# Kernel tuning notes

Measured on AMD Instinct MI355X. Metric: run time of the kernel, lower is better.

Reference implementation:

```python
import jax, jax.numpy as jnp
import numpy as np

EPS = 1e-5


def _instance_norm(a):
    # InstanceNorm2d(affine=False): normalize each [*, ch] plane over last two dims
    mu = jnp.mean(a, axis=(-2, -1), keepdims=True)
    var = jnp.var(a, axis=(-2, -1), keepdims=True)  # biased, matches torch
    return (a - mu) * jax.lax.rsqrt(var + EPS)


def setup_inputs() -> dict:
    key = jax.random.key(0)
    ks = jax.random.split(key, 10)
    B, N, C, H = 8, 4096, 128, 8
    HC = C * H
    s = 0.02
    return {
        "emb": jax.random.normal(ks[0], (B, N, C), jnp.float32),
        "wq_uu": jax.random.normal(ks[1], (HC, C), jnp.float32) * s,
        "wk_uu": jax.random.normal(ks[2], (HC, C), jnp.float32) * s,
        "wv_uu": jax.random.normal(ks[3], (HC, C), jnp.float32) * s,
        "wq_lu": jax.random.normal(ks[4], (HC, C), jnp.float32) * s,
        "wk_lu": jax.random.normal(ks[5], (HC, C), jnp.float32) * s,
        "wv_lu": jax.random.normal(ks[6], (HC, C), jnp.float32) * s,
        "wo_u": jax.random.normal(ks[7], (C, HC), jnp.float32) * s,
        "wo_l": jax.random.normal(ks[8], (C, HC), jnp.float32) * s,
    }


def reference(emb, wq_uu, wk_uu, wv_uu, wq_lu, wk_lu, wv_lu, wo_u, wo_l):
    B, N, C = emb.shape
    HC = wq_uu.shape[0]
    H = HC // C
    b = B // 2
    emb_l, emb_u = emb[:b], emb[b:]

    def heads(x, w):  # [b,N,C] @ [HC,C]^T -> [b,H,N,C]
        return (x @ w.T).reshape(b, N, H, C).transpose(0, 2, 1, 3)

    # ---- branch u_u: channel attention within unlabeled half ----
    Q = heads(emb_u, wq_uu)  # [b,H,N,C]
    K = heads(emb_u, wk_uu)  # [b,H,N,C]
    V = heads(emb_u, wv_uu)  # [b,H,N,C]
    attn = jnp.einsum('bhnc,bhnd->bhcd', Q, K)          # Q^T K : [b,H,C,C]
    sim = jax.nn.softmax(_instance_norm(attn), axis=3)
    ctx = jnp.einsum('bhcd,bhnd->bhcn', sim, V)         # [b,H,C,N]
    # permute(0,3,2,1) then flatten (C,H) -> c-major, h-minor
    ctx = ctx.transpose(0, 3, 2, 1).reshape(b, N, HC)
    O_u = ctx @ wo_u.T                                   # [b,N,C]

    # ---- branch l_u: labeled queries attend over concat-of-batch unlabeled K/V ----
    Q2 = emb_l @ wq_lu.T                                 # [b,N,HC]
    K2 = (emb_u @ wk_lu.T).transpose(1, 0, 2).reshape(N, b * HC)  # 'b n c -> n (b c)'
    V2 = (emb_u @ wv_lu.T).transpose(1, 0, 2).reshape(N, b * HC)
    attn2 = jnp.einsum('bnc,nd->bcd', Q2, K2)            # [b,HC,b*HC] (single head)
    sim2 = jax.nn.softmax(_instance_norm(attn2), axis=2)
    ctx2 = jnp.einsum('bcd,nd->bnc', sim2, V2)           # [b,N,HC]
    O_l = ctx2 @ wo_l.T                                  # [b,N,C]

    return jnp.concatenate([O_l, O_u], axis=0)
```

## Files before the change

kernel.cpp:

```cpp
#include <hip/hip_runtime.h>
#include <hip/hip_bf16.h>

using bf16 = __hip_bfloat16;
typedef __attribute__((ext_vector_type(8))) short bf16x8;
typedef __attribute__((ext_vector_type(4))) float f32x4;

static __device__ __forceinline__ void storeC(float* p, float v) { *p = v; }
static __device__ __forceinline__ void storeC(bf16* p, float v) { *p = __float2bfloat16(v); }

static __device__ __forceinline__ void gl2lds16(const bf16* g, bf16* l)
{
    __builtin_amdgcn_global_load_lds(
        (const __attribute__((address_space(1))) unsigned int*)g,
        (__attribute__((address_space(3))) unsigned int*)l, 16, 0, 0);
}

static __device__ __forceinline__ void stage_tile(const bf16* gtile, int ld, bf16* ltile, int w, int lane)
{
    const bf16* g0 = gtile + (long)(w * 32 + (lane >> 2)) * ld + ((lane & 3) << 3);
    gl2lds16(g0, ltile + (w * 32) * 32);
    gl2lds16(g0 + (long)16 * ld, ltile + (w * 32 + 16) * 32);
}

template <typename TC, bool ATOMIC>
__global__ __launch_bounds__(256) void gemm_mfma_nt(
    const bf16* __restrict__ A0, const bf16* __restrict__ B0, TC* __restrict__ C0,
    int K, int lda, int ldb, int ldc, int zdiv,
    long sAhi, long sAlo, long sBhi, long sBlo, long sChi, long sClo)
{
    __shared__ bf16 As[2][4096];
    __shared__ bf16 Bs[2][4096];
    const int z = blockIdx.z;
    const bf16* A = A0 + (long)(z / zdiv) * sAhi + (long)(z % zdiv) * sAlo + (long)blockIdx.y * 128 * lda;
    const bf16* B = B0 + (long)(z / zdiv) * sBhi + (long)(z % zdiv) * sBlo + (long)blockIdx.x * 128 * ldb;
    TC*       C = C0 + (long)(z / zdiv) * sChi + (long)(z % zdiv) * sClo;

    const int t = threadIdx.x, lane = t & 63, w = t >> 6;
    const int wm = w >> 1, wn = w & 1;

    f32x4 acc[4][4] = {};

    stage_tile(A, lda, &As[0][0], w, lane);
    stage_tile(B, ldb, &Bs[0][0], w, lane);

    const int KT = K >> 5;
    for (int kt = 0; kt < KT; ++kt) {
        __syncthreads();
        const int cur = kt & 1;
        if (kt + 1 < KT) {
            stage_tile(A + (kt + 1) * 32, lda, &As[cur ^ 1][0], w, lane);
            stage_tile(B + (kt + 1) * 32, ldb, &Bs[cur ^ 1][0], w, lane);
        }
        const int kofs = (lane >> 4) << 3;
        bf16x8 av[4], bv[4];
#pragma unroll
        for (int i = 0; i < 4; ++i)
            av[i] = *(const bf16x8*)&As[cur][(wm * 64 + i * 16 + (lane & 15)) * 32 + kofs];
#pragma unroll
        for (int j = 0; j < 4; ++j)
            bv[j] = *(const bf16x8*)&Bs[cur][(wn * 64 + j * 16 + (lane & 15)) * 32 + kofs];
#pragma unroll
        for (int i = 0; i < 4; ++i)
#pragma unroll
            for (int j = 0; j < 4; ++j)
                acc[i][j] = __builtin_amdgcn_mfma_f32_16x16x32_bf16(av[i], bv[j], acc[i][j], 0, 0, 0);
    }

    const int r0 = blockIdx.y * 128 + wm * 64;
    const int c0 = blockIdx.x * 128 + wn * 64;
    const int lcol = lane & 15, lrow = (lane >> 4) << 2;
#pragma unroll
    for (int i = 0; i < 4; ++i)
#pragma unroll
        for (int j = 0; j < 4; ++j) {
            const int row = r0 + i * 16 + lrow;
            const int col = c0 + j * 16 + lcol;
#pragma unroll
            for (int r = 0; r < 4; ++r) {
                if constexpr (ATOMIC)
                    atomicAdd(&C[(long)(row + r) * ldc + col], acc[i][j][r]);
                else
                    storeC(&C[(long)(row + r) * ldc + col], acc[i][j][r]);
            }
        }
}

template <typename TC, bool STATS>
__global__ __launch_bounds__(512, 2) void gemm_mfma_nt256(
    const bf16* __restrict__ A0, const bf16* __restrict__ B0, TC* __restrict__ C0,
    int K, int lda, int ldb, int ldc, long sA, long sB, long sC, float* __restrict__ red)
{
    extern __shared__ bf16 lds[];
    const int z = blockIdx.z;
    const bf16* A = A0 + (long)z * sA + (long)blockIdx.y * 256 * lda;
    const bf16* B = B0 + (long)z * sB + (long)blockIdx.x * 256 * ldb;
    TC*       C = C0 + (long)z * sC;

    const int t = threadIdx.x, lane = t & 63, w = t >> 6;
    const int wm = w >> 2, wn = w & 3;
    const int lr = lane & 15, lg = lane >> 4;

    f32x4 acc[8][4] = {};
    const int KT = K >> 5;

    const int srow = t >> 2, spc = t & 3;
    auto STAGE_A = [&](int c) {
        bf16* base = lds + (c & 3) * 16384;
        const bf16* Ag = A + c * 32;
        const int r0 = srow, r1 = srow + 128;
        gl2lds16(Ag + (long)r0 * lda + ((spc ^ ((r0 >> 1) & 3)) << 3), base + w * 512);
        gl2lds16(Ag + (long)r1 * lda + ((spc ^ ((r1 >> 1) & 3)) << 3), base + 4096 + w * 512);
    };
    auto STAGE_B = [&](int c) {
        bf16* base = lds + (c & 3) * 16384 + 8192;
        const bf16* Bg = B + c * 32;
        const int r0 = srow, r1 = srow + 128;
        gl2lds16(Bg + (long)r0 * ldb + ((spc ^ ((r0 >> 1) & 3)) << 3), base + w * 512);
        gl2lds16(Bg + (long)r1 * ldb + ((spc ^ ((r1 >> 1) & 3)) << 3), base + 4096 + w * 512);
    };

    if (KT > 0) { STAGE_A(0); STAGE_B(0); }
    if (KT > 1) { STAGE_A(1); STAGE_B(1); }
    if (KT > 2) { STAGE_A(2); STAGE_B(2); }

    for (int c = 0; c < KT; ++c) {
        const int rem = KT - 1 - c;
        if (rem >= 2)      asm volatile("s_waitcnt vmcnt(8)" ::: "memory");
        else if (rem == 1) asm volatile("s_waitcnt vmcnt(4)" ::: "memory");
        else               asm volatile("s_waitcnt vmcnt(0)" ::: "memory");
        __builtin_amdgcn_s_barrier();
        asm volatile("" ::: "memory");

        const bf16* Ab = lds + (c & 3) * 16384;
        const bf16* Bb = Ab + 8192;
        const bool pf = (c + 3 < KT);

        bf16x8 bfrag[4], afragA[4];
#pragma unroll
        for (int j = 0; j < 4; ++j) {
            const int r = wn * 64 + j * 16 + lr;
            bfrag[j] = *(const bf16x8*)&Bb[r * 32 + ((lg ^ ((r >> 1) & 3)) << 3)];
        }
#pragma unroll
        for (int i = 0; i < 4; ++i) {
            const int r = wm * 128 + i * 16 + lr;
            afragA[i] = *(const bf16x8*)&Ab[r * 32 + ((lg ^ ((r >> 1) & 3)) << 3)];
        }
        if (pf) STAGE_A(c + 3);
        __builtin_amdgcn_s_barrier();
        __builtin_amdgcn_s_setprio(1);
#pragma unroll
        for (int i = 0; i < 4; ++i)
#pragma unroll
            for (int j = 0; j < 4; ++j)
                acc[i][j] = __builtin_amdgcn_mfma_f32_16x16x32_bf16(afragA[i], bfrag[j], acc[i][j], 0, 0, 0);
        __builtin_amdgcn_s_setprio(0);
        __builtin_amdgcn_s_barrier();

        bf16x8 afragB[4];
#pragma unroll
        for (int i = 0; i < 4; ++i) {
            const int r = wm * 128 + (4 + i) * 16 + lr;
            afragB[i] = *(const bf16x8*)&Ab[r * 32 + ((lg ^ ((r >> 1) & 3)) << 3)];
        }
        if (pf) STAGE_B(c + 3);
        __builtin_amdgcn_s_barrier();
        __builtin_amdgcn_s_setprio(1);
#pragma unroll
        for (int i = 0; i < 4; ++i)
#pragma unroll
            for (int j = 0; j < 4; ++j)
                acc[4 + i][j] = __builtin_amdgcn_mfma_f32_16x16x32_bf16(afragB[i], bfrag[j], acc[4 + i][j], 0, 0, 0);
        __builtin_amdgcn_s_setprio(0);
        __builtin_amdgcn_s_barrier();
    }

    const int r0 = blockIdx.y * 256 + wm * 128 + (lg << 2);
    const int c0 = blockIdx.x * 256 + wn * 64 + lr;
#pragma unroll
    for (int i = 0; i < 8; ++i)
#pragma unroll
        for (int j = 0; j < 4; ++j) {
#pragma unroll
            for (int rr = 0; rr < 4; ++rr)
                storeC(&C[(long)(r0 + i * 16 + rr) * ldc + (c0 + j * 16)], acc[i][j][rr]);
        }

    if constexpr (STATS) {
        float s1 = 0.f, s2 = 0.f;
#pragma unroll
        for (int i = 0; i < 8; ++i)
#pragma unroll
            for (int j = 0; j < 4; ++j)
#pragma unroll
                for (int rr = 0; rr < 4; ++rr) {
                    float v = acc[i][j][rr];
                    s1 += v; s2 += v * v;
                }
#pragma unroll
        for (int o = 32; o > 0; o >>= 1) { s1 += __shfl_xor(s1, o); s2 += __shfl_xor(s2, o); }
        __syncthreads();
        float* rb = (float*)lds;
        if (lane == 0) { rb[w] = s1; rb[8 + w] = s2; }
        __syncthreads();
        if (t == 0) {
            float a = 0.f, b = 0.f;
#pragma unroll
            for (int i = 0; i < 8; ++i) { a += rb[i]; b += rb[8 + i]; }
            atomicAdd(&red[z * 2], a);
            atomicAdd(&red[z * 2 + 1], b);
        }
    }
}

__global__ __launch_bounds__(256) void prep(
    const float* __restrict__ emb,
    const float* w0, const float* w1, const float* w2, const float* w3,
    const float* w4, const float* w5, const float* w6,
    const float* __restrict__ wo_u,
    bf16* __restrict__ embB, bf16* __restrict__ wB, bf16* __restrict__ woUrB,
    float* __restrict__ attnU, float* __restrict__ red2)
{
    const int b = blockIdx.x;
    if (b < 2048 || (b >= 2048 && b < 2496)) {
        const float* in;
        bf16* out;
        int i;
        if (b < 2048) {
            in = emb; out = embB;
            i = (b * 256 + threadIdx.x) * 8;
        } else {
            const int sub = b - 2048;
            const float* srcs[7] = {w0, w1, w2, w3, w4, w5, w6};
            in = srcs[sub >> 6];
            out = wB + (long)(sub >> 6) * 131072;
            i = ((sub & 63) * 256 + threadIdx.x) * 8;
        }
        float4 a = *(const float4*)(in + i);
        float4 c = *(const float4*)(in + i + 4);
        union { bf16 h[8]; uint4 u; } pk;
        pk.h[0] = __float2bfloat16(a.x); pk.h[1] = __float2bfloat16(a.y);
        pk.h[2] = __float2bfloat16(a.z); pk.h[3] = __float2bfloat16(a.w);
        pk.h[4] = __float2bfloat16(c.x); pk.h[5] = __float2bfloat16(c.y);
        pk.h[6] = __float2bfloat16(c.z); pk.h[7] = __float2bfloat16(c.w);
        *(uint4*)(out + i) = pk.u;
    } else if (b < 3008) {
        int i = (b - 2496) * 256 + threadIdx.x;
        int j = i >> 10, col = i & 1023;
        int h = col >> 7, cc = col & 127;
        woUrB[i] = __float2bfloat16(wo_u[j * 1024 + cc * 8 + h]);
    } else if (b < 3520) {
        int i = ((b - 3008) * 256 + threadIdx.x) * 4;
        *(float4*)(attnU + i) = float4{0.f, 0.f, 0.f, 0.f};
    } else {
        if (threadIdx.x < 8) red2[threadIdx.x] = 0.f;
    }
}

__global__ __launch_bounds__(256) void stats_bh(const float* __restrict__ x, float* __restrict__ stats)
{
    const float* p = x + (long)blockIdx.x * 16384;
    float s1 = 0.f, s2 = 0.f;
    for (int i = threadIdx.x; i < 16384; i += 256) { float v = p[i]; s1 += v; s2 += v * v; }
    __shared__ float r1[256], r2[256];
    int t = threadIdx.x;
    r1[t] = s1; r2[t] = s2; __syncthreads();
    for (int o = 128; o > 0; o >>= 1) {
        if (t < o) { r1[t] += r1[t + o]; r2[t] += r2[t + o]; }
        __syncthreads();
    }
    if (t == 0) {
        float mu = r1[0] * (1.f / 16384.f);
        float var = r2[0] * (1.f / 16384.f) - mu * mu;
        stats[blockIdx.x * 2] = mu;
        stats[blockIdx.x * 2 + 1] = rsqrtf(var + 1e-5f);
    }
}

__global__ __launch_bounds__(128) void softmax_row128(const float* __restrict__ attn,
                                                      const float* __restrict__ stats,
                                                      bf16* __restrict__ out)
{
    const int row = blockIdx.x;
    const int bh = row >> 7;
    const float mu = stats[bh * 2], rs = stats[bh * 2 + 1];
    const float* p = attn + (long)row * 128;
    const int t = threadIdx.x;
    float x = (p[t] - mu) * rs;
    float m = x;
#pragma unroll
    for (int o = 32; o > 0; o >>= 1) m = fmaxf(m, __shfl_xor(m, o));
    __shared__ float sm[2], ss[2];
    if ((t & 63) == 0) sm[t >> 6] = m;
    __syncthreads();
    m = fmaxf(sm[0], sm[1]);
    float e = expf(x - m);
    float s = e;
#pragma unroll
    for (int o = 32; o > 0; o >>= 1) s += __shfl_xor(s, o);
    if ((t & 63) == 0) ss[t >> 6] = s;
    __syncthreads();
    s = ss[0] + ss[1];
    out[(long)row * 128 + t] = __float2bfloat16(e / s);
}

__global__ __launch_bounds__(256) void softmax_row4096(const float* __restrict__ attn2,
                                                       const float* __restrict__ red,
                                                       bf16* __restrict__ out)
{
    const int row = blockIdx.x;
    const int b = row >> 10;
    const float inv = 1.f / 4194304.f;
    float mu = red[b * 2] * inv;
    float var = red[b * 2 + 1] * inv - mu * mu;
    float rs = rsqrtf(var + 1e-5f);
    const float* p = attn2 + (long)row * 4096;
    bf16* q = out + (long)row * 4096;
    const int t = threadIdx.x;
    float v[16];
    float mx = -3.0e38f;
#pragma unroll
    for (int i = 0; i < 16; ++i) { float u = (p[i * 256 + t] - mu) * rs; v[i] = u; mx = fmaxf(mx, u); }
#pragma unroll
    for (int o = 32; o > 0; o >>= 1) mx = fmaxf(mx, __shfl_xor(mx, o));
    __shared__ float sm[4], ss[4];
    if ((t & 63) == 0) sm[t >> 6] = mx;
    __syncthreads();
    mx = fmaxf(fmaxf(sm[0], sm[1]), fmaxf(sm[2], sm[3]));
    float s = 0.f;
#pragma unroll
    for (int i = 0; i < 16; ++i) { v[i] = expf(v[i] - mx); s += v[i]; }
#pragma unroll
    for (int o = 32; o > 0; o >>= 1) s += __shfl_xor(s, o);
    if ((t & 63) == 0) ss[t >> 6] = s;
    __syncthreads();
    s = ss[0] + ss[1] + ss[2] + ss[3];
    float r = 1.f / s;
#pragma unroll
    for (int i = 0; i < 16; ++i) q[i * 256 + t] = __float2bfloat16(v[i] * r);
}

extern "C" void kernel_launch(void* const* d_in, const int* in_sizes, int n_in,
                              void* d_out, int out_size, void* d_ws, size_t ws_size,
                              hipStream_t stream)
{
    const float* emb   = (const float*)d_in[0];
    const float* wq_uu = (const float*)d_in[1];
    const float* wk_uu = (const float*)d_in[2];
    const float* wv_uu = (const float*)d_in[3];
    const float* wq_lu = (const float*)d_in[4];
    const float* wk_lu = (const float*)d_in[5];
    const float* wv_lu = (const float*)d_in[6];
    const float* wo_u  = (const float*)d_in[7];
    const float* wo_l  = (const float*)d_in[8];
    float* out = (float*)d_out;

    hipFuncSetAttribute(reinterpret_cast<const void*>(&gemm_mfma_nt256<float, true>),
                        hipFuncAttributeMaxDynamicSharedMemorySize, 131072);
    hipFuncSetAttribute(reinterpret_cast<const void*>(&gemm_mfma_nt256<bf16, false>),
                        hipFuncAttributeMaxDynamicSharedMemorySize, 131072);

    const long U = 16777216;
    bf16*  ws     = (bf16*)d_ws;
    bf16*  slot0  = ws;
    bf16*  slot1  = ws + U;
    float* attn2F = (float*)(ws + 2 * U);
    float* attnU  = attn2F;
    bf16*  VuB    = (bf16*)attn2F;
    bf16*  ctx2B  = (bf16*)attn2F;
    bf16*  embB   = ws + 4 * U;
    bf16*  wB     = embB + 4194304;
    bf16*  wqUU  = wB;
    bf16*  wqLU  = wB + 262144;
    bf16*  wvUU  = wB + 524288;
    bf16*  wvLU  = wB + 655360;
    bf16*  woLB  = wB + 786432;
    bf16*  woUrB = wB + 917504;
    bf16*  simU   = wB + 1048576;
    float* statsF = (float*)(simU + 524288);
    float* statsU = statsF;
    float* red2   = statsF + 64;
    bf16*  ctxUB  = (bf16*)(statsF + 128);

    bf16* embB_l = embB;
    bf16* embB_u = embB + 2097152;

    dim3 blk(256);

    prep<<<dim3(3521), blk, 0, stream>>>(
        emb, wq_uu, wk_uu, wq_lu, wk_lu, wv_uu, wv_lu, wo_l, wo_u,
        embB, wB, woUrB, attnU, red2);

    gemm_mfma_nt<bf16, false><<<dim3(32, 8, 8), blk, 0, stream>>>(
        wqUU, embB_u, slot0, 128, 128, 128, 4096,
        4, 131072, 0, 0, 524288, 16777216, 4194304);

    gemm_mfma_nt<float, true><<<dim3(1, 1, 256), blk, 0, stream>>>(
        slot0, slot1, attnU, 512, 4096, 4096, 128,
        8, 524288, 512, 524288, 512, 16384, 0);

    stats_bh<<<dim3(32), blk, 0, stream>>>(attnU, statsU);
    softmax_row128<<<dim3(4096), dim3(128), 0, stream>>>(attnU, statsU, simU);

    gemm_mfma_nt<bf16, false><<<dim3(8, 32, 4), blk, 0, stream>>>(
        embB_u, wvUU, VuB, 128, 128, 128, 1024, 1, 524288, 0, 0, 0, 4194304, 0);

    gemm_mfma_nt<bf16, false><<<dim3(1, 32, 32), blk, 0, stream>>>(
        VuB, simU, ctxUB, 128, 1024, 128, 1024,
        8, 4194304, 128, 131072, 16384, 4194304, 128);

    gemm_mfma_nt<bf16, false><<<dim3(32, 8, 8), blk, 0, stream>>>(
        wqLU, embB_l, slot0, 128, 128, 128, 4096,
        4, 131072, 0, 2097152, 524288, 16777216, 4194304);

    gemm_mfma_nt256<float, true><<<dim3(16, 4, 4), dim3(512), 131072, stream>>>(
        slot0, slot1, attn2F, 4096, 4096, 4096, 4096,
        4194304, 0, 4194304, red2);

    softmax_row4096<<<dim3(4096), blk, 0, stream>>>(attn2F, red2, slot0);

    gemm_mfma_nt<bf16, false><<<dim3(8, 32, 4), blk, 0, stream>>>(
        embB_u, wvLU, slot1, 128, 128, 128, 4096, 1, 524288, 0, 0, 0, 1024, 0);

    gemm_mfma_nt256<bf16, false><<<dim3(4, 16, 4), dim3(512), 131072, stream>>>(
        slot1, slot0, ctx2B, 4096, 4096, 4096, 1024,
        0, 4194304, 4194304, nullptr);

    gemm_mfma_nt<float, false><<<dim3(1, 128, 2), blk, 0, stream>>>(
        ctx2B, woLB, out, 1024, 1024, 1024, 128,
        1, (long)(ctxUB - ctx2B), 0, 131072, 0, 2097152, 0);
}
```

Baseline: 500.5 us.

## Reassociate output projection through softmax matrices and fuse softmax stages

The output projections are reassociated: Wo·sim is computed first as small weight-sized products (W2u, W2l), so the large ctx2 GEMM over N×HC is replaced by a V·W2 product with split-K partials summed in a reduce kernel. The u-branch stats and softmax are merged into one kernel that also writes a transposed sim. The l-branch softmax is split into row-stats and transposed-write kernels. The 256 GEMM pipeline is simplified to one combined A/B stage per iteration with fewer barriers. The aim is to cut the FLOPs and memory traffic of the ctx2 path, at the cost of extra kernels and an added partial-sum reduction.

```diff
diff --git a/kernel.cpp b/kernel.cpp
--- a/kernel.cpp
+++ b/kernel.cpp
@@ -104,24 +104,22 @@
     const int KT = K >> 5;
 
     const int srow = t >> 2, spc = t & 3;
-    auto STAGE_A = [&](int c) {
+    auto STAGE = [&](int c) {
         bf16* base = lds + (c & 3) * 16384;
         const bf16* Ag = A + c * 32;
-        const int r0 = srow, r1 = srow + 128;
-        gl2lds16(Ag + (long)r0 * lda + ((spc ^ ((r0 >> 1) & 3)) << 3), base + w * 512);
-        gl2lds16(Ag + (long)r1 * lda + ((spc ^ ((r1 >> 1) & 3)) << 3), base + 4096 + w * 512);
+        const bf16* Bg = B + c * 32;
+        int r0 = srow, r1 = srow + 128;
+        int c0 = (spc ^ ((r0 >> 1) & 3)) << 3;
+        int c1 = (spc ^ ((r1 >> 1) & 3)) << 3;
+        gl2lds16(Ag + (long)r0 * lda + c0, base + w * 512);
+        gl2lds16(Ag + (long)r1 * lda + c1, base + 4096 + w * 512);
+        gl2lds16(Bg + (long)r0 * ldb + c0, base + 8192 + w * 512);
+        gl2lds16(Bg + (long)r1 * ldb + c1, base + 12288 + w * 512);
     };
-    auto STAGE_B = [&](int c) {
-        bf16* base = lds + (c & 3) * 16384 + 8192;
-        const bf16* Bg = B + c * 32;
-        const int r0 = srow, r1 = srow + 128;
-        gl2lds16(Bg + (long)r0 * ldb + ((spc ^ ((r0 >> 1) & 3)) << 3), base + w * 512);
-        gl2lds16(Bg + (long)r1 * ldb + ((spc ^ ((r1 >> 1) & 3)) << 3), base + 4096 + w * 512);
-    };
-
-    if (KT > 0) { STAGE_A(0); STAGE_B(0); }
-    if (KT > 1) { STAGE_A(1); STAGE_B(1); }
-    if (KT > 2) { STAGE_A(2); STAGE_B(2); }
+
+    if (KT > 0) STAGE(0);
+    if (KT > 1) STAGE(1);
+    if (KT > 2) STAGE(2);
 
     for (int c = 0; c < KT; ++c) {
         const int rem = KT - 1 - c;
@@ -130,49 +128,28 @@
         else               asm volatile("s_waitcnt vmcnt(0)" ::: "memory");
         __builtin_amdgcn_s_barrier();
         asm volatile("" ::: "memory");
+        if (c + 3 < KT) STAGE(c + 3);
 
         const bf16* Ab = lds + (c & 3) * 16384;
         const bf16* Bb = Ab + 8192;
-        const bool pf = (c + 3 < KT);
-
-        bf16x8 bfrag[4], afragA[4];
+        bf16x8 bfrag[4], afrag[8];
 #pragma unroll
         for (int j = 0; j < 4; ++j) {
             const int r = wn * 64 + j * 16 + lr;
             bfrag[j] = *(const bf16x8*)&Bb[r * 32 + ((lg ^ ((r >> 1) & 3)) << 3)];
         }
 #pragma unroll
-        for (int i = 0; i < 4; ++i) {
+        for (int i = 0; i < 8; ++i) {
             const int r = wm * 128 + i * 16 + lr;
-            afragA[i] = *(const bf16x8*)&Ab[r * 32 + ((lg ^ ((r >> 1) & 3)) << 3)];
-        }
-        if (pf) STAGE_A(c + 3);
-        __builtin_amdgcn_s_barrier();
+            afrag[i] = *(const bf16x8*)&Ab[r * 32 + ((lg ^ ((r >> 1) & 3)) << 3)];
+        }
         __builtin_amdgcn_s_setprio(1);
 #pragma unroll
-        for (int i = 0; i < 4; ++i)
+        for (int i = 0; i < 8; ++i)
 #pragma unroll
             for (int j = 0; j < 4; ++j)
-                acc[i][j] = __builtin_amdgcn_mfma_f32_16x16x32_bf16(afragA[i], bfrag[j], acc[i][j], 0, 0, 0);
+                acc[i][j] = __builtin_amdgcn_mfma_f32_16x16x32_bf16(afrag[i], bfrag[j], acc[i][j], 0, 0, 0);
         __builtin_amdgcn_s_setprio(0);
-        __builtin_amdgcn_s_barrier();
-
-        bf16x8 afragB[4];
-#pragma unroll
-        for (int i = 0; i < 4; ++i) {
-            const int r = wm * 128 + (4 + i) * 16 + lr;
-            afragB[i] = *(const bf16x8*)&Ab[r * 32 + ((lg ^ ((r >> 1) & 3)) << 3)];
-        }
-        if (pf) STAGE_B(c + 3);
-        __builtin_amdgcn_s_barrier();
-        __builtin_amdgcn_s_setprio(1);
-#pragma unroll
-        for (int i = 0; i < 4; ++i)
-#pragma unroll
-            for (int j = 0; j < 4; ++j)
-                acc[4 + i][j] = __builtin_amdgcn_mfma_f32_16x16x32_bf16(afragB[i], bfrag[j], acc[4 + i][j], 0, 0, 0);
-        __builtin_amdgcn_s_setprio(0);
-        __builtin_amdgcn_s_barrier();
     }
 
     const int r0 = blockIdx.y * 256 + wm * 128 + (lg << 2);
@@ -222,7 +199,7 @@
     float* __restrict__ attnU, float* __restrict__ red2)
 {
     const int b = blockIdx.x;
-    if (b < 2048 || (b >= 2048 && b < 2496)) {
+    if (b < 2496) {
         const float* in;
         bf16* out;
         int i;
@@ -257,70 +234,69 @@
     }
 }
 
-__global__ __launch_bounds__(256) void stats_bh(const float* __restrict__ x, float* __restrict__ stats)
-{
-    const float* p = x + (long)blockIdx.x * 16384;
+__global__ __launch_bounds__(256) void softmaxU_fused(const float* __restrict__ attnU,
+                                                      bf16* __restrict__ simUT)
+{
+    extern __shared__ float sm[];
+    float* tile = sm;
+    float* rowinv = sm + 128 * 129;
+    float* rbuf = rowinv + 128;
+    const int bh = blockIdx.x;
+    const float* p = attnU + (long)bh * 16384;
+    const int t = threadIdx.x;
+
     float s1 = 0.f, s2 = 0.f;
-    for (int i = threadIdx.x; i < 16384; i += 256) { float v = p[i]; s1 += v; s2 += v * v; }
-    __shared__ float r1[256], r2[256];
-    int t = threadIdx.x;
-    r1[t] = s1; r2[t] = s2; __syncthreads();
-    for (int o = 128; o > 0; o >>= 1) {
-        if (t < o) { r1[t] += r1[t + o]; r2[t] += r2[t + o]; }
-        __syncthreads();
-    }
-    if (t == 0) {
-        float mu = r1[0] * (1.f / 16384.f);
-        float var = r2[0] * (1.f / 16384.f) - mu * mu;
-        stats[blockIdx.x * 2] = mu;
-        stats[blockIdx.x * 2 + 1] = rsqrtf(var + 1e-5f);
-    }
-}
-
-__global__ __launch_bounds__(128) void softmax_row128(const float* __restrict__ attn,
-                                                      const float* __restrict__ stats,
-                                                      bf16* __restrict__ out)
-{
-    const int row = blockIdx.x;
-    const int bh = row >> 7;
-    const float mu = stats[bh * 2], rs = stats[bh * 2 + 1];
-    const float* p = attn + (long)row * 128;
-    const int t = threadIdx.x;
-    float x = (p[t] - mu) * rs;
-    float m = x;
-#pragma unroll
-    for (int o = 32; o > 0; o >>= 1) m = fmaxf(m, __shfl_xor(m, o));
-    __shared__ float sm[2], ss[2];
-    if ((t & 63) == 0) sm[t >> 6] = m;
+    for (int i = t; i < 16384; i += 256) {
+        float v = p[i];
+        tile[(i >> 7) * 129 + (i & 127)] = v;
+        s1 += v; s2 += v * v;
+    }
+#pragma unroll
+    for (int o = 32; o > 0; o >>= 1) { s1 += __shfl_xor(s1, o); s2 += __shfl_xor(s2, o); }
+    if ((t & 63) == 0) { rbuf[t >> 6] = s1; rbuf[4 + (t >> 6)] = s2; }
     __syncthreads();
-    m = fmaxf(sm[0], sm[1]);
-    float e = expf(x - m);
-    float s = e;
-#pragma unroll
-    for (int o = 32; o > 0; o >>= 1) s += __shfl_xor(s, o);
-    if ((t & 63) == 0) ss[t >> 6] = s;
+    const float mu = (rbuf[0] + rbuf[1] + rbuf[2] + rbuf[3]) * (1.f / 16384.f);
+    const float m2 = (rbuf[4] + rbuf[5] + rbuf[6] + rbuf[7]) * (1.f / 16384.f);
+    const float rs = rsqrtf(m2 - mu * mu + 1e-5f);
+
+    if (t < 128) {
+        float* row = tile + t * 129;
+        float mx = -3.0e38f;
+        for (int d = 0; d < 128; ++d) mx = fmaxf(mx, row[d]);
+        float s = 0.f;
+        for (int d = 0; d < 128; ++d) { float e = expf((row[d] - mx) * rs); row[d] = e; s += e; }
+        rowinv[t] = 1.f / s;
+    }
     __syncthreads();
-    s = ss[0] + ss[1];
-    out[(long)row * 128 + t] = __float2bfloat16(e / s);
-}
-
-__global__ __launch_bounds__(256) void softmax_row4096(const float* __restrict__ attn2,
-                                                       const float* __restrict__ red,
-                                                       bf16* __restrict__ out)
-{
-    const int row = blockIdx.x;
-    const int b = row >> 10;
+    {
+        const int d = t >> 1, ch = (t & 1) * 64;
+        bf16* q = simUT + (long)bh * 16384 + d * 128 + ch;
+        for (int i = 0; i < 64; i += 2) {
+            float a = tile[(ch + i) * 129 + d] * rowinv[ch + i];
+            float b = tile[(ch + i + 1) * 129 + d] * rowinv[ch + i + 1];
+            union { bf16 h[2]; unsigned u; } pk;
+            pk.h[0] = __float2bfloat16(a); pk.h[1] = __float2bfloat16(b);
+            *(unsigned*)(q + i) = pk.u;
+        }
+    }
+}
+
+__global__ __launch_bounds__(256) void sm2_rowstats(const float* __restrict__ attn2,
+                                                    const float* __restrict__ red,
+                                                    float* __restrict__ rowstat)
+{
+    const int r = blockIdx.x;
+    const int b = r >> 10;
     const float inv = 1.f / 4194304.f;
-    float mu = red[b * 2] * inv;
-    float var = red[b * 2 + 1] * inv - mu * mu;
-    float rs = rsqrtf(var + 1e-5f);
-    const float* p = attn2 + (long)row * 4096;
-    bf16* q = out + (long)row * 4096;
+    const float mu = red[b * 2] * inv;
+    const float var = red[b * 2 + 1] * inv - mu * mu;
+    const float rs = rsqrtf(var + 1e-5f);
+    const float* p = attn2 + (long)r * 4096;
     const int t = threadIdx.x;
     float v[16];
     float mx = -3.0e38f;
 #pragma unroll
-    for (int i = 0; i < 16; ++i) { float u = (p[i * 256 + t] - mu) * rs; v[i] = u; mx = fmaxf(mx, u); }
+    for (int i = 0; i < 16; ++i) { v[i] = p[i * 256 + t]; mx = fmaxf(mx, v[i]); }
 #pragma unroll
     for (int o = 32; o > 0; o >>= 1) mx = fmaxf(mx, __shfl_xor(mx, o));
     __shared__ float sm[4], ss[4];
@@ -329,15 +305,69 @@
     mx = fmaxf(fmaxf(sm[0], sm[1]), fmaxf(sm[2], sm[3]));
     float s = 0.f;
 #pragma unroll
-    for (int i = 0; i < 16; ++i) { v[i] = expf(v[i] - mx); s += v[i]; }
+    for (int i = 0; i < 16; ++i) s += expf((v[i] - mx) * rs);
 #pragma unroll
     for (int o = 32; o > 0; o >>= 1) s += __shfl_xor(s, o);
     if ((t & 63) == 0) ss[t >> 6] = s;
     __syncthreads();
-    s = ss[0] + ss[1] + ss[2] + ss[3];
-    float r = 1.f / s;
-#pragma unroll
-    for (int i = 0; i < 16; ++i) q[i * 256 + t] = __float2bfloat16(v[i] * r);
+    if (t == 0) {
+        s = ss[0] + ss[1] + ss[2] + ss[3];
+        rowstat[r * 2] = mx;
+        rowstat[r * 2 + 1] = 1.f / s;
+    }
+}
+
+__global__ __launch_bounds__(256) void sm2_transpose(const float* __restrict__ attn2,
+                                                     const float* __restrict__ red,
+                                                     const float* __restrict__ rowstat,
+                                                     bf16* __restrict__ sim2T)
+{
+    extern __shared__ float tile[];
+    const int dt = blockIdx.x, ct = blockIdx.y, b = blockIdx.z;
+    const float inv = 1.f / 4194304.f;
+    const float mu = red[b * 2] * inv;
+    const float var = red[b * 2 + 1] * inv - mu * mu;
+    const float rs = rsqrtf(var + 1e-5f);
+    const int t = threadIdx.x;
+    const float* in = attn2 + (long)b * 4194304 + (long)(ct * 128) * 4096 + dt * 128;
+    {
+        const int c = t >> 1, dh = (t & 1) * 64;
+        const float2 st = *(const float2*)&rowstat[(b * 1024 + ct * 128 + c) * 2];
+        const float mx = st.x, is = st.y;
+        const float* src = in + (long)c * 4096 + dh;
+        float* dst = tile + c * 129 + dh;
+        for (int i = 0; i < 64; i += 4) {
+            float4 x = *(const float4*)(src + i);
+            dst[i]     = expf((x.x - mx) * rs) * is;
+            dst[i + 1] = expf((x.y - mx) * rs) * is;
+            dst[i + 2] = expf((x.z - mx) * rs) * is;
+            dst[i + 3] = expf((x.w - mx) * rs) * is;
+        }
+    }
+    __syncthreads();
+    {
+        const int d = t >> 1, ch = (t & 1) * 64;
+        bf16* q = sim2T + (long)b * 4194304 + (long)(dt * 128 + d) * 1024 + ct * 128 + ch;
+        for (int i = 0; i < 64; i += 2) {
+            union { bf16 h[2]; unsigned u; } pk;
+            pk.h[0] = __float2bfloat16(tile[(ch + i) * 129 + d]);
+            pk.h[1] = __float2bfloat16(tile[(ch + i + 1) * 129 + d]);
+            *(unsigned*)(q + i) = pk.u;
+        }
+    }
+}
+
+__global__ __launch_bounds__(256) void reduce4(const float* __restrict__ pOl,
+                                               const float* __restrict__ pOu,
+                                               float* __restrict__ out)
+{
+    const long i = ((long)blockIdx.x * 256 + threadIdx.x) * 4;
+    const float* src = (i < 2097152) ? (pOl + i) : (pOu + (i - 2097152));
+    f32x4 a = *(const f32x4*)src;
+    a += *(const f32x4*)(src + 2097152);
+    a += *(const f32x4*)(src + 4194304);
+    a += *(const f32x4*)(src + 6291456);
+    *(f32x4*)(out + i) = a;
 }
 
 extern "C" void kernel_launch(void* const* d_in, const int* in_sizes, int n_in,
@@ -357,18 +387,22 @@
 
     hipFuncSetAttribute(reinterpret_cast<const void*>(&gemm_mfma_nt256<float, true>),
                         hipFuncAttributeMaxDynamicSharedMemorySize, 131072);
-    hipFuncSetAttribute(reinterpret_cast<const void*>(&gemm_mfma_nt256<bf16, false>),
-                        hipFuncAttributeMaxDynamicSharedMemorySize, 131072);
+    hipFuncSetAttribute(reinterpret_cast<const void*>(&softmaxU_fused),
+                        hipFuncAttributeMaxDynamicSharedMemorySize, 66592);
+    hipFuncSetAttribute(reinterpret_cast<const void*>(&sm2_transpose),
+                        hipFuncAttributeMaxDynamicSharedMemorySize, 66048);
 
     const long U = 16777216;
-    bf16*  ws     = (bf16*)d_ws;
-    bf16*  slot0  = ws;
-    bf16*  slot1  = ws + U;
-    float* attn2F = (float*)(ws + 2 * U);
+    bf16*  ws0    = (bf16*)d_ws;
+    bf16*  slot0  = ws0;
+    bf16*  slot1  = ws0 + U;
+    float* attn2F = (float*)(ws0 + 2 * U);
     float* attnU  = attn2F;
     bf16*  VuB    = (bf16*)attn2F;
-    bf16*  ctx2B  = (bf16*)attn2F;
-    bf16*  embB   = ws + 4 * U;
+    float* pOu    = attn2F + 8388608;
+    float* pOl    = (float*)slot0;
+    bf16*  sim2T  = slot0;
+    bf16*  embB   = ws0 + 4 * U;
     bf16*  wB     = embB + 4194304;
     bf16*  wqUU  = wB;
     bf16*  wqLU  = wB + 262144;
@@ -376,11 +410,12 @@
     bf16*  wvLU  = wB + 655360;
     bf16*  woLB  = wB + 786432;
     bf16*  woUrB = wB + 917504;
-    bf16*  simU   = wB + 1048576;
-    float* statsF = (float*)(simU + 524288);
-    float* statsU = statsF;
-    float* red2   = statsF + 64;
-    bf16*  ctxUB  = (bf16*)(statsF + 128);
+    bf16*  simUT = wB + 1048576;
+    bf16*  W2uB  = wB + 1572864;
+    bf16*  W2lB  = wB + 2097152;
+    float* statsF = (float*)(wB + 4194304);
+    float* red2   = statsF;
+    float* rowstat = statsF + 8;
 
     bf16* embB_l = embB;
     bf16* embB_u = embB + 2097152;
@@ -399,15 +434,7 @@
         slot0, slot1, attnU, 512, 4096, 4096, 128,
         8, 524288, 512, 524288, 512, 16384, 0);
 
-    stats_bh<<<dim3(32), blk, 0, stream>>>(attnU, statsU);
-    softmax_row128<<<dim3(4096), dim3(128), 0, stream>>>(attnU, statsU, simU);
-
-    gemm_mfma_nt<bf16, false><<<dim3(8, 32, 4), blk, 0, stream>>>(
-        embB_u, wvUU, VuB, 128, 128, 128, 1024, 1, 524288, 0, 0, 0, 4194304, 0);
-
-    gemm_mfma_nt<bf16, false><<<dim3(1, 32, 32), blk, 0, stream>>>(
-        VuB, simU, ctxUB, 128, 1024, 128, 1024,
-        8, 4194304, 128, 131072, 16384, 4194304, 128);
+    softmaxU_fused<<<dim3(32), blk, 66592, stream>>>(attnU, simUT);
 
     gemm_mfma_nt<bf16, false><<<dim3(32, 8, 8), blk, 0, stream>>>(
         wqLU, embB_l, slot0, 128, 128, 128, 4096,
@@ -417,16 +444,30 @@
         slot0, slot1, attn2F, 4096, 4096, 4096, 4096,
         4194304, 0, 4194304, red2);
 
-    softmax_row4096<<<dim3(4096), blk, 0, stream>>>(attn2F, red2, slot0);
+    sm2_rowstats<<<dim3(4096), blk, 0, stream>>>(attn2F, red2, rowstat);
+    sm2_transpose<<<dim3(32, 8, 4), blk, 66048, stream>>>(attn2F, red2, rowstat, sim2T);
 
     gemm_mfma_nt<bf16, false><<<dim3(8, 32, 4), blk, 0, stream>>>(
         embB_u, wvLU, slot1, 128, 128, 128, 4096, 1, 524288, 0, 0, 0, 1024, 0);
 
-    gemm_mfma_nt256<bf16, false><<<dim3(4, 16, 4), dim3(512), 131072, stream>>>(
-        slot1, slot0, ctx2B, 4096, 4096, 4096, 1024,
-        0, 4194304, 4194304, nullptr);
-
-    gemm_mfma_nt<float, false><<<dim3(1, 128, 2), blk, 0, stream>>>(
-        ctx2B, woLB, out, 1024, 1024, 1024, 128,
-        1, (long)(ctxUB - ctx2B), 0, 131072, 0, 2097152, 0);
-}
+    gemm_mfma_nt<bf16, false><<<dim3(8, 32, 4), blk, 0, stream>>>(
+        embB_u, wvUU, VuB, 128, 128, 128, 1024, 1, 524288, 0, 0, 0, 4194304, 0);
+
+    gemm_mfma_nt<bf16, false><<<dim3(1, 1, 32), blk, 0, stream>>>(
+        woUrB, simUT, W2uB, 128, 1024, 128, 1024,
+        8, 0, 128, 131072, 16384, 131072, 128);
+
+    gemm_mfma_nt<bf16, false><<<dim3(32, 1, 4), blk, 0, stream>>>(
+        woLB, sim2T, W2lB, 1024, 1024, 1024, 4096,
+        1, 0, 0, 4194304, 0, 524288, 0);
+
+    gemm_mfma_nt<float, false><<<dim3(1, 32, 16), blk, 0, stream>>>(
+        VuB, W2uB, pOu, 256, 1024, 1024, 128,
+        4, 256, 4194304, 256, 131072, 2097152, 524288);
+
+    gemm_mfma_nt<float, false><<<dim3(1, 32, 16), blk, 0, stream>>>(
+        slot1, W2lB, pOl, 1024, 4096, 4096, 128,
+        4, 1024, 0, 1024, 524288, 2097152, 524288);
+
+    reduce4<<<dim3(4096), blk, 0, stream>>>(pOl, pOu, out);
+}
```

After: 451.1 us. -9.9%, faster.
